# Kernel tuning notes

Measured on AMD Instinct MI355X. Metric: run time of the kernel, lower is better.

## Reference

```python
import jax, jax.numpy as jnp
import numpy as np

B, M, N, P, Q, GRID, DIM = 8, 64, 64, 3, 3, 512, 3


def _clamped_knots(n_ctrl, p):
    # clamped uniform knot vector of length n_ctrl + p + 1
    interior = np.linspace(0.0, 1.0, n_ctrl - p + 1)[1:-1]
    return np.concatenate([np.zeros(p + 1), interior, np.ones(p + 1)]).astype(np.float32)


def _find_span(u, knots, n_ctrl, p):
    spans = np.searchsorted(knots, u, side='right') - 1
    return np.clip(spans, p, n_ctrl - 1).astype(np.int32)


def _basis_funs(u, spans, knots, p):
    # Cox-de Boor (Algorithm A2.2, The NURBS Book), vectorized over the grid
    G = u.shape[0]
    Nb = np.zeros((G, p + 1), np.float32)
    Nb[:, 0] = 1.0
    left = np.zeros((G, p + 1), np.float32)
    right = np.zeros((G, p + 1), np.float32)
    for j in range(1, p + 1):
        left[:, j] = u - knots[spans + 1 - j]
        right[:, j] = knots[spans + j] - u
        saved = np.zeros(G, np.float32)
        for r in range(j):
            temp = Nb[:, r] / (right[:, r + 1] + left[:, j - r])
            Nb[:, r] = saved + right[:, r + 1] * temp
            saved = left[:, j - r] * temp
        Nb[:, j] = saved
    return Nb


def setup_inputs() -> dict:
    key = jax.random.key(0)
    k1, k2 = jax.random.split(key)
    U = _clamped_knots(M, P)
    V = _clamped_knots(N, Q)
    u = np.linspace(0.0, 1.0, GRID, dtype=np.float32)
    v = np.linspace(0.0, 1.0, GRID, dtype=np.float32)
    uspan = _find_span(u, U, M, P)
    vspan = _find_span(v, V, N, Q)
    Nu = _basis_funs(u, uspan, U, P)
    Nv = _basis_funs(v, vspan, V, Q)
    xyz = jax.random.normal(k1, (B, M, N, DIM), jnp.float32)
    w = jax.random.uniform(k2, (B, M, N, 1), jnp.float32, minval=0.5, maxval=1.5)
    ctrl_pts = jnp.concatenate([xyz * w, w], axis=-1)  # homogeneous [B,M,N,4]
    return {
        'ctrl_pts': ctrl_pts,
        'uspan': jnp.asarray(uspan),
        'vspan': jnp.asarray(vspan),
        'Nu': jnp.asarray(Nu),
        'Nv': jnp.asarray(Nv),
    }


def reference(ctrl_pts, uspan, vspan, Nu, Nv):
    # surfaces[b,i,j,:] = sum_{r,s} Nu[i,r] Nv[j,s] ctrl[b, uspan[i]-P+r, vspan[j]-Q+s, :]
    idx_u = uspan[:, None] - P + jnp.arange(P + 1)   # [G, P+1]
    idx_v = vspan[:, None] - Q + jnp.arange(Q + 1)   # [G, Q+1]
    pts_u = ctrl_pts[:, idx_u]                        # [B, G, P+1, N, 4] gather
    Su = jnp.einsum('gr,bgrnd->bgnd', Nu, pts_u)      # [B, G, N, 4]
    pts_v = Su[:, :, idx_v]                           # [B, G, G, Q+1, 4] gather
    Sw = jnp.einsum('hs,bghsd->bghd', Nv, pts_v)      # [B, G, G, 4] homogeneous
    return Sw[..., :DIM] / Sw[..., DIM:DIM + 1]       # perspective divide
```

## Files before the change

### kernel.cpp

```cpp
#include <hip/hip_runtime.h>

#define GRID_PTS 512
#define M_CTRL   64
#define N_CTRL   64

__global__ __launch_bounds__(128) void surfeval_kernel(
    const float4* __restrict__ ctrl,
    const int*    __restrict__ uspan,
    const int*    __restrict__ vspan,
    const float4* __restrict__ Nu,
    const float4* __restrict__ Nv,
    float*        __restrict__ out)
{
    __shared__ float4 Su[N_CTRL];
    __shared__ float  obuf[GRID_PTS * 3];

    const int blk = blockIdx.x;
    const int g   = blk & (GRID_PTS - 1);
    const int b   = blk >> 9;
    const int t   = threadIdx.x;

    if (t < N_CTRL) {
        const int    iu = uspan[g] - 3;
        const float4 nu = Nu[g];
        const float4* cp = ctrl + ((size_t)b * M_CTRL + iu) * N_CTRL + t;
        const float4 c0 = cp[0 * N_CTRL];
        const float4 c1 = cp[1 * N_CTRL];
        const float4 c2 = cp[2 * N_CTRL];
        const float4 c3 = cp[3 * N_CTRL];
        float4 s;
        s.x = nu.x * c0.x + nu.y * c1.x + nu.z * c2.x + nu.w * c3.x;
        s.y = nu.x * c0.y + nu.y * c1.y + nu.z * c2.y + nu.w * c3.y;
        s.z = nu.x * c0.z + nu.y * c1.z + nu.z * c2.z + nu.w * c3.z;
        s.w = nu.x * c0.w + nu.y * c1.w + nu.z * c2.w + nu.w * c3.w;
        Su[t] = s;
    }
    __syncthreads();

#pragma unroll
    for (int j = 0; j < 4; ++j) {
        const int    h  = j * 128 + t;
        const int    iv = vspan[h] - 3;
        const float4 nv = Nv[h];
        const float4 a0 = Su[iv + 0];
        const float4 a1 = Su[iv + 1];
        const float4 a2 = Su[iv + 2];
        const float4 a3 = Su[iv + 3];
        const float sx = nv.x * a0.x + nv.y * a1.x + nv.z * a2.x + nv.w * a3.x;
        const float sy = nv.x * a0.y + nv.y * a1.y + nv.z * a2.y + nv.w * a3.y;
        const float sz = nv.x * a0.z + nv.y * a1.z + nv.z * a2.z + nv.w * a3.z;
        const float sw = nv.x * a0.w + nv.y * a1.w + nv.z * a2.w + nv.w * a3.w;
        const float inv = __builtin_amdgcn_rcpf(sw);
        obuf[h * 3 + 0] = sx * inv;
        obuf[h * 3 + 1] = sy * inv;
        obuf[h * 3 + 2] = sz * inv;
    }
    __syncthreads();

    const float4* ob4 = (const float4*)obuf;
    float4* op = (float4*)(out + (size_t)blk * (GRID_PTS * 3));
    op[t      ] = ob4[t      ];
    op[t + 128] = ob4[t + 128];
    op[t + 256] = ob4[t + 256];
}

extern "C" void kernel_launch(void* const* d_in, const int* in_sizes, int n_in,
                              void* d_out, int out_size, void* d_ws, size_t ws_size,
                              hipStream_t stream) {
    const float4* ctrl  = (const float4*)d_in[0];
    const int*    uspan = (const int*)d_in[1];
    const int*    vspan = (const int*)d_in[2];
    const float4* Nu    = (const float4*)d_in[3];
    const float4* Nv    = (const float4*)d_in[4];
    float*        out   = (float*)d_out;

    const int blocks = 8 * GRID_PTS;
    surfeval_kernel<<<blocks, 128, 0, stream>>>(ctrl, uspan, vspan, Nu, Nv, out);
}
```

Before: 72.36 us.

## Process four u-rows per block with 512 threads, reusing per-thread v-basis loads

Each block now covers four consecutive u grid rows with 512 threads instead of one row with 128. Every thread loads its own vspan/Nv entry once and reuses it across the four rows. Ctrl loads for the four rows are done in parallel, one thread per row and column. This cuts per-block overhead and redundant basis loads and gives larger contiguous output stores. In exchange it uses more shared memory per block (about 28KB) and launches fewer blocks (1024).

```diff
diff --git a/kernel.cpp b/kernel.cpp
--- a/kernel.cpp
+++ b/kernel.cpp
@@ -3,8 +3,9 @@
 #define GRID_PTS 512
 #define M_CTRL   64
 #define N_CTRL   64
+#define ROWS     4
 
-__global__ __launch_bounds__(128) void surfeval_kernel(
+__global__ __launch_bounds__(512) void surfeval_kernel(
     const float4* __restrict__ ctrl,
     const int*    __restrict__ uspan,
     const int*    __restrict__ vspan,
@@ -12,18 +13,24 @@
     const float4* __restrict__ Nv,
     float*        __restrict__ out)
 {
-    __shared__ float4 Su[N_CTRL];
-    __shared__ float  obuf[GRID_PTS * 3];
+    __shared__ float4 Su[ROWS][N_CTRL];
+    __shared__ float  obuf[ROWS * GRID_PTS * 3];
 
-    const int blk = blockIdx.x;
-    const int g   = blk & (GRID_PTS - 1);
-    const int b   = blk >> 9;
-    const int t   = threadIdx.x;
+    const int blk   = blockIdx.x;
+    const int b     = blk >> 7;
+    const int gbase = (blk & 127) << 2;
+    const int t     = threadIdx.x;
 
-    if (t < N_CTRL) {
-        const int    iu = uspan[g] - 3;
+    const int    iv = vspan[t] - 3;
+    const float4 nv = Nv[t];
+
+    if (t < ROWS * N_CTRL) {
+        const int row = t >> 6;
+        const int n   = t & 63;
+        const int g   = gbase + row;
+        const int iu  = uspan[g] - 3;
         const float4 nu = Nu[g];
-        const float4* cp = ctrl + ((size_t)b * M_CTRL + iu) * N_CTRL + t;
+        const float4* cp = ctrl + ((size_t)b * M_CTRL + iu) * N_CTRL + n;
         const float4 c0 = cp[0 * N_CTRL];
         const float4 c1 = cp[1 * N_CTRL];
         const float4 c2 = cp[2 * N_CTRL];
@@ -33,35 +40,33 @@
         s.y = nu.x * c0.y + nu.y * c1.y + nu.z * c2.y + nu.w * c3.y;
         s.z = nu.x * c0.z + nu.y * c1.z + nu.z * c2.z + nu.w * c3.z;
         s.w = nu.x * c0.w + nu.y * c1.w + nu.z * c2.w + nu.w * c3.w;
-        Su[t] = s;
+        Su[row][n] = s;
     }
     __syncthreads();
 
 #pragma unroll
-    for (int j = 0; j < 4; ++j) {
-        const int    h  = j * 128 + t;
-        const int    iv = vspan[h] - 3;
-        const float4 nv = Nv[h];
-        const float4 a0 = Su[iv + 0];
-        const float4 a1 = Su[iv + 1];
-        const float4 a2 = Su[iv + 2];
-        const float4 a3 = Su[iv + 3];
+    for (int r = 0; r < ROWS; ++r) {
+        const float4 a0 = Su[r][iv + 0];
+        const float4 a1 = Su[r][iv + 1];
+        const float4 a2 = Su[r][iv + 2];
+        const float4 a3 = Su[r][iv + 3];
         const float sx = nv.x * a0.x + nv.y * a1.x + nv.z * a2.x + nv.w * a3.x;
         const float sy = nv.x * a0.y + nv.y * a1.y + nv.z * a2.y + nv.w * a3.y;
         const float sz = nv.x * a0.z + nv.y * a1.z + nv.z * a2.z + nv.w * a3.z;
         const float sw = nv.x * a0.w + nv.y * a1.w + nv.z * a2.w + nv.w * a3.w;
         const float inv = __builtin_amdgcn_rcpf(sw);
-        obuf[h * 3 + 0] = sx * inv;
-        obuf[h * 3 + 1] = sy * inv;
-        obuf[h * 3 + 2] = sz * inv;
+        float* ob = obuf + r * (GRID_PTS * 3) + t * 3;
+        ob[0] = sx * inv;
+        ob[1] = sy * inv;
+        ob[2] = sz * inv;
     }
     __syncthreads();
 
     const float4* ob4 = (const float4*)obuf;
-    float4* op = (float4*)(out + (size_t)blk * (GRID_PTS * 3));
-    op[t      ] = ob4[t      ];
-    op[t + 128] = ob4[t + 128];
-    op[t + 256] = ob4[t + 256];
+    float4* op = (float4*)(out + (size_t)(b * GRID_PTS + gbase) * (GRID_PTS * 3));
+#pragma unroll
+    for (int k = 0; k < 3; ++k)
+        op[t + k * 512] = ob4[t + k * 512];
 }
 
 extern "C" void kernel_launch(void* const* d_in, const int* in_sizes, int n_in,
@@ -74,6 +79,6 @@
     const float4* Nv    = (const float4*)d_in[4];
     float*        out   = (float*)d_out;
 
-    const int blocks = 8 * GRID_PTS;
-    surfeval_kernel<<<blocks, 128, 0, stream>>>(ctrl, uspan, vspan, Nu, Nv, out);
+    const int blocks = 8 * (GRID_PTS / ROWS);
+    surfeval_kernel<<<blocks, 512, 0, stream>>>(ctrl, uspan, vspan, Nu, Nv, out);
 }
```

Measured after the change: 71.17 us. About the same (-1.6%).
